# Optimization experiments

Hardware: AMD Instinct MI355X
Metric: run time of the kernel (lower is better)

The kernel has to match this reference:

```python
import jax, jax.numpy as jnp
import numpy as np

CMIN, CMAX = -1024.0, 1016.0  # clamp(min=-2**10, max=2**10 - 8) after every op
BRIGHT_F = 1.9   # 1.0 + linspace(0, 0.9, 11)[10]
COLOR_F = 1.9    # 1.0 + linspace(0, 0.9, 11)[10]


def _brightness_dct(x, f):
    # pixel-domain multiplicative brightness; DCT is linear -> scale all coeffs
    return x * f


def _contrast_dct(x, f):
    # pixel contrast: (p - mean)*f + mean.
    # In DCT: AC coeffs scale by f; DC coeff blends toward per-channel mean DC.
    dc_mean = jnp.mean(x[..., 0, 0], axis=(-2, -1), keepdims=True)  # [C,1,1]
    out = x * f
    out = out.at[..., 0, 0].add((1.0 - f) * dc_mean)
    return out


def setup_inputs() -> dict:
    key = jax.random.key(0)
    k1, k2 = jax.random.split(key)
    # luma: [C=1, Hblocks, Wblocks, 8, 8]; chroma 4:2:0: [C=2, H/2, W/2, 8, 8]
    y = jax.random.normal(k1, (1, 512, 512, 8, 8), dtype=jnp.float32) * 100.0
    c = jax.random.normal(k2, (2, 256, 256, 8, 8), dtype=jnp.float32) * 100.0
    return {"y": y, "c": c}


def reference(y, c):
    clamp = lambda t: jnp.clip(t, CMIN, CMAX)
    # dct_prep(mode='start') treated as identity; initial clamp as in forward()
    y = clamp(y)
    c = clamp(c)
    # op 1: Brightness on luma (coeff[0]); both planes clamped after each op
    y = clamp(_brightness_dct(y, BRIGHT_F))
    c = clamp(c)
    # op 2: Color = contrast on chroma (coeff[1])
    c = clamp(_contrast_dct(c, COLOR_F))
    y = clamp(y)
    # dct_prep(mode='end') treated as identity
    return y, c
```

## Files before the change

kernel.cpp:

```cpp
#include <hip/hip_runtime.h>

#define CMIN -1024.0f
#define CMAX 1016.0f
#define NBLK 512
#define NTHR 256

__device__ __forceinline__ float clampv(float x) {
    return fminf(fmaxf(x, CMIN), CMAX);
}

__global__ void __launch_bounds__(NTHR)
fused_all(const float4* __restrict__ y4, const float4* __restrict__ c4,
          const float*  __restrict__ c,  float4* __restrict__ outy,
          float4* __restrict__ outc, float* __restrict__ ws,
          unsigned* __restrict__ done,
          int ynvec, int cnvec, int dc_per_ch, float inv_count) {
    const int tid  = threadIdx.x;
    const int gtid = blockIdx.x * NTHR + tid;

    {
        float v = clampv(c[(size_t)gtid * 64]);
        #pragma unroll
        for (int off = 32; off > 0; off >>= 1)
            v += __shfl_down(v, off, 64);
        __shared__ float smem[NTHR / 64];
        if ((tid & 63) == 0) smem[tid >> 6] = v;
        __syncthreads();
        if (tid == 0) {
            float s = 0.f;
            #pragma unroll
            for (int w = 0; w < NTHR / 64; ++w) s += smem[w];
            const int ch = (gtid < dc_per_ch) ? 0 : 1;
            atomicAdd(&ws[ch], s);
            __threadfence();
            atomicAdd(done, 1u);
        }
    }

    for (int i = gtid; i < ynvec; i += NBLK * NTHR) {
        float4 v = y4[i];
        v.x = clampv(clampv(v.x) * 1.9f);
        v.y = clampv(clampv(v.y) * 1.9f);
        v.z = clampv(clampv(v.z) * 1.9f);
        v.w = clampv(clampv(v.w) * 1.9f);
        outy[i] = v;
    }

    __shared__ float sdc[2];
    if (tid == 0) {
        while (__hip_atomic_load(done, __ATOMIC_ACQUIRE,
                                 __HIP_MEMORY_SCOPE_AGENT) < (unsigned)NBLK) {}
        sdc[0] = __hip_atomic_load(&ws[0], __ATOMIC_RELAXED,
                                   __HIP_MEMORY_SCOPE_AGENT) * inv_count;
        sdc[1] = __hip_atomic_load(&ws[1], __ATOMIC_RELAXED,
                                   __HIP_MEMORY_SCOPE_AGENT) * inv_count;
    }
    __syncthreads();
    const float adj0 = -0.9f * sdc[0];
    const float adj1 = -0.9f * sdc[1];

    const int chalf = cnvec >> 1;
    for (int i = gtid; i < cnvec; i += NBLK * NTHR) {
        float4 v = c4[i];
        float4 r;
        r.x = clampv(v.x) * 1.9f;
        r.y = clampv(v.y) * 1.9f;
        r.z = clampv(v.z) * 1.9f;
        r.w = clampv(v.w) * 1.9f;
        if ((i & 15) == 0)
            r.x += (i < chalf) ? adj0 : adj1;
        r.x = clampv(r.x);
        r.y = clampv(r.y);
        r.z = clampv(r.z);
        r.w = clampv(r.w);
        outc[i] = r;
    }
}

extern "C" void kernel_launch(void* const* d_in, const int* in_sizes, int n_in,
                              void* d_out, int out_size, void* d_ws, size_t ws_size,
                              hipStream_t stream) {
    const float* y = (const float*)d_in[0];
    const float* c = (const float*)d_in[1];
    float* out = (float*)d_out;

    const int yN = in_sizes[0];
    const int cN = in_sizes[1];

    float* ws = (float*)d_ws;
    unsigned* done = (unsigned*)(ws + 2);

    hipMemsetAsync(ws, 0, 16, stream);

    const int ynvec = yN / 4;
    const int cnvec = cN / 4;
    const int dc_per_ch = cN / 64 / 2;
    const float inv_count = 1.0f / (float)dc_per_ch;

    fused_all<<<NBLK, NTHR, 0, stream>>>(
        (const float4*)y, (const float4*)c, c,
        (float4*)out, (float4*)(out + yN),
        ws, done, ynvec, cnvec, dc_per_ch, inv_count);
}
```

Before: 202.8 us.

## Quadruple grid size and hand out DC-reduction chunks through an atomic ticket

Raises the grid from 512 to 2048 blocks so more waves are in flight for the streaming luma and chroma passes. The per-channel DC sum is now split into 512 chunks claimed through an atomic ticket counter, so only blocks that are actually resident do reduction work before every block spin-waits on the done counter. Both streaming loops get an unroll hint, and the DC-lane test is hoisted because the stride is a multiple of 16. The cost is extra atomic traffic and per-block syncs, and the grid-wide spin still depends on the ticket scheme to avoid waiting on blocks that are not yet scheduled.

```diff
diff --git a/kernel.cpp b/kernel.cpp
--- a/kernel.cpp
+++ b/kernel.cpp
@@ -2,8 +2,10 @@
 
 #define CMIN -1024.0f
 #define CMAX 1016.0f
-#define NBLK 512
+#define NBLK 2048
 #define NTHR 256
+#define GSTRIDE (NBLK * NTHR)
+#define DC_CHUNKS 512
 
 __device__ __forceinline__ float clampv(float x) {
     return fminf(fmaxf(x, CMIN), CMAX);
@@ -13,31 +15,44 @@
 fused_all(const float4* __restrict__ y4, const float4* __restrict__ c4,
           const float*  __restrict__ c,  float4* __restrict__ outy,
           float4* __restrict__ outc, float* __restrict__ ws,
-          unsigned* __restrict__ done,
           int ynvec, int cnvec, int dc_per_ch, float inv_count) {
     const int tid  = threadIdx.x;
     const int gtid = blockIdx.x * NTHR + tid;
 
-    {
-        float v = clampv(c[(size_t)gtid * 64]);
+    unsigned* ticket = (unsigned*)(ws + 2);
+    unsigned* done   = (unsigned*)(ws + 3);
+
+    __shared__ unsigned s_chunk;
+    __shared__ float smem[NTHR / 64];
+    for (;;) {
+        if (tid == 0)
+            s_chunk = __hip_atomic_fetch_add(ticket, 1u, __ATOMIC_RELAXED,
+                                             __HIP_MEMORY_SCOPE_AGENT);
+        __syncthreads();
+        unsigned chunk = s_chunk;
+        if (chunk >= DC_CHUNKS) break;
+        int dc_idx = chunk * NTHR + tid;
+        float v = clampv(c[(size_t)dc_idx * 64]);
         #pragma unroll
         for (int off = 32; off > 0; off >>= 1)
             v += __shfl_down(v, off, 64);
-        __shared__ float smem[NTHR / 64];
         if ((tid & 63) == 0) smem[tid >> 6] = v;
         __syncthreads();
         if (tid == 0) {
             float s = 0.f;
             #pragma unroll
             for (int w = 0; w < NTHR / 64; ++w) s += smem[w];
-            const int ch = (gtid < dc_per_ch) ? 0 : 1;
+            const int ch = (dc_idx < dc_per_ch) ? 0 : 1;
             atomicAdd(&ws[ch], s);
             __threadfence();
-            atomicAdd(done, 1u);
+            __hip_atomic_fetch_add(done, 1u, __ATOMIC_RELEASE,
+                                   __HIP_MEMORY_SCOPE_AGENT);
         }
+        __syncthreads();
     }
 
-    for (int i = gtid; i < ynvec; i += NBLK * NTHR) {
+    #pragma unroll 2
+    for (int i = gtid; i < ynvec; i += GSTRIDE) {
         float4 v = y4[i];
         v.x = clampv(clampv(v.x) * 1.9f);
         v.y = clampv(clampv(v.y) * 1.9f);
@@ -49,7 +64,7 @@
     __shared__ float sdc[2];
     if (tid == 0) {
         while (__hip_atomic_load(done, __ATOMIC_ACQUIRE,
-                                 __HIP_MEMORY_SCOPE_AGENT) < (unsigned)NBLK) {}
+                                 __HIP_MEMORY_SCOPE_AGENT) < DC_CHUNKS) {}
         sdc[0] = __hip_atomic_load(&ws[0], __ATOMIC_RELAXED,
                                    __HIP_MEMORY_SCOPE_AGENT) * inv_count;
         sdc[1] = __hip_atomic_load(&ws[1], __ATOMIC_RELAXED,
@@ -60,14 +75,16 @@
     const float adj1 = -0.9f * sdc[1];
 
     const int chalf = cnvec >> 1;
-    for (int i = gtid; i < cnvec; i += NBLK * NTHR) {
+    const bool is_dc = ((gtid & 15) == 0);
+    #pragma unroll 2
+    for (int i = gtid; i < cnvec; i += GSTRIDE) {
         float4 v = c4[i];
         float4 r;
         r.x = clampv(v.x) * 1.9f;
         r.y = clampv(v.y) * 1.9f;
         r.z = clampv(v.z) * 1.9f;
         r.w = clampv(v.w) * 1.9f;
-        if ((i & 15) == 0)
+        if (is_dc)
             r.x += (i < chalf) ? adj0 : adj1;
         r.x = clampv(r.x);
         r.y = clampv(r.y);
@@ -88,7 +105,6 @@
     const int cN = in_sizes[1];
 
     float* ws = (float*)d_ws;
-    unsigned* done = (unsigned*)(ws + 2);
 
     hipMemsetAsync(ws, 0, 16, stream);
 
@@ -100,5 +116,5 @@
     fused_all<<<NBLK, NTHR, 0, stream>>>(
         (const float4*)y, (const float4*)c, c,
         (float4*)out, (float4*)(out + yN),
-        ws, done, ynvec, cnvec, dc_per_ch, inv_count);
+        ws, ynvec, cnvec, dc_per_ch, inv_count);
 }
```

New measurement: 313.7 us. 1.55x slower.
